# Performance work log

Hardware: AMD Instinct MI355X
Metric: run time of the kernel (lower is better)

The kernel has to match this reference:

```python
import jax, jax.numpy as jnp
import numpy as np

THRESH = 1.0
BETA = 0.9
SG_ALPHA = 2.0  # snntorch ATan surrogate default alpha

@jax.custom_vjp
def spike(u):
    # Heaviside fire: 1 where membrane exceeds threshold
    return (u > 0).astype(u.dtype)

def _spike_fwd(u):
    return spike(u), u

def _spike_bwd(u, g):
    # snntorch ATan surrogate gradient: (alpha/2) / (1 + (pi/2*alpha*u)^2)
    return (g * (SG_ALPHA / 2) / (1.0 + (jnp.pi / 2 * SG_ALPHA * u) ** 2),)

spike.defvjp(_spike_fwd, _spike_bwd)

def setup_inputs() -> dict:
    key = jax.random.key(0)
    k1, k2, k3 = jax.random.split(key, 3)
    T, B, N_IN, N1, N2 = 64, 256, 2048, 1024, 1024
    # Bernoulli(0.2) binary input spike trains
    input_spikes = (jax.random.uniform(k1, (T, B, N_IN)) < 0.2).astype(jnp.float32)
    s = 1.0 / np.sqrt(N_IN)  # nn.Linear default init range
    W1 = jax.random.uniform(k2, (N1, N_IN), minval=-s, maxval=s, dtype=jnp.float32)
    W2 = jax.random.uniform(k3, (N2, N_IN), minval=-s, maxval=s, dtype=jnp.float32)
    return {"input_spikes": input_spikes, "W1": W1, "W2": W2}

def _lif_layer(cur_seq, beta, thr):
    # cur_seq: [T, B, N] post-synaptic currents. snntorch Leaky, reset-by-subtraction:
    #   reset_t = H(mem_{t-1} - thr); mem_t = beta*mem_{t-1} + cur_t - reset_t*thr; spk_t = H(mem_t - thr)
    def step(mem, cur):
        reset = spike(mem - thr)
        mem = beta * mem + cur - reset * thr
        spk = spike(mem - thr)
        return mem, (spk, mem)
    init_mem = jnp.zeros_like(cur_seq[0])
    _, (spk_rec, mem_rec) = jax.lax.scan(step, init_mem, cur_seq)
    return spk_rec, mem_rec  # each [T, B, N]

def reference(input_spikes, W1, W2):
    # Source quirk (faithful): every fc layer consumes the raw input spikes.
    cur1 = jnp.einsum('tbi,ni->tbn', input_spikes, W1)  # [T,B,N1]
    cur2 = jnp.einsum('tbi,ni->tbn', input_spikes, W2)  # [T,B,N2]
    spk1, mem1 = _lif_layer(cur1, BETA, THRESH)
    spk2, mem2 = _lif_layer(cur2, BETA, THRESH)
    return spk1, mem1, spk2, mem2
```

## Files before the change

### kernel.cpp

```cpp
#include <hip/hip_runtime.h>
#include <hip/hip_bf16.h>
#include <stdint.h>


#define REGION 16777216
#define BN_ELEMS 262144
#define FLAG_EPS 3e-4f

typedef __attribute__((ext_vector_type(4))) int v4i;

typedef __attribute__((address_space(1))) const void gvoid_t;
typedef __attribute__((address_space(3))) void svoid_t;

__device__ __forceinline__ void gload_lds16(const void* g, void* l) {
  __builtin_amdgcn_global_load_lds((gvoid_t*)g, (svoid_t*)l, 16, 0, 0);
}

__global__ void prep_kernel(const float* __restrict__ spikes, int* __restrict__ s4,
                            unsigned long long* __restrict__ maskR,
                            int* __restrict__ count,
                            const float* __restrict__ W1, const float* __restrict__ W2,
                            signed char* __restrict__ Bp) {
  int blk = blockIdx.x;
  if (blk < 2048) {
    int id = blk * 256 + threadIdx.x;
    if (id == 0) *count = 0;
    int row = id >> 5, c = id & 31;
    const float4* p = (const float4*)(spikes + (long long)row * 2048 + c * 64);
    unsigned long long m = 0;
    int* sd = s4 + (row * 2048 + c * 64) / 4;
#pragma unroll
    for (int q = 0; q < 16; ++q) {
      float4 v = p[q];
      int b0 = (v.x != 0.f), b1 = (v.y != 0.f), b2 = (v.z != 0.f), b3 = (v.w != 0.f);
      sd[q] = b0 | (b1 << 8) | (b2 << 16) | (b3 << 24);
      m |= (unsigned long long)b0 << (4 * q);
      m |= (unsigned long long)b1 << (4 * q + 1);
      m |= (unsigned long long)b2 << (4 * q + 2);
      m |= (unsigned long long)b3 << (4 * q + 3);
    }
    maskR[(long long)row * 32 + c] = m;
  } else {
    int idx = (blk - 2048) * 256 + threadIdx.x;
    int n = idx >> 11, k = idx & 2047;
    float w = (n < 1024) ? W1[n * 2048 + k] : W2[(n - 1024) * 2048 + k];
    int V = (int)rintf(w * 1048576.0f);
    int d0 = ((V + 128) & 255) - 128;
    int d1 = (V - d0) >> 8;
    signed char* row = Bp + (long long)n * 4096;
    row[k]        = (signed char)d1;
    row[2048 + k] = (signed char)d0;
  }
}

__global__ __launch_bounds__(512) void gemm_snn(const signed char* __restrict__ S,
                                                const signed char* __restrict__ Bp,
                                                float* __restrict__ out) {
  __shared__ __align__(16) signed char As[3 * 8192];
  __shared__ __align__(16) signed char Bs0[3 * 8192];
  __shared__ __align__(16) signed char Bs1[3 * 8192];
  const int tid = threadIdx.x;
  const int wv = tid >> 6, ln = tid & 63;

  int bid = blockIdx.x;
  int swz = (bid & 7) * 128 + (bid >> 3);
  const int bm = swz >> 3;
  const int bn = swz & 7;
  const int wr = wv >> 2, wc = wv & 3;

  const int srow = wv * 16 + (ln >> 2);
  const int scolb = ((ln & 3) ^ ((srow >> 1) & 3)) * 16;
  const signed char* aSrc  = S  + (long long)(bm * 128 + srow) * 2048 + scolb;
  const signed char* b0Src = Bp + (long long)(bn * 128 + srow) * 4096 + scolb;
  const signed char* b1Src = Bp + (long long)(1024 + bn * 128 + srow) * 4096 + scolb;
  const int ldsW = wv * 1024;

  const int l15 = ln & 15, l4 = ln >> 4;
  int aOff[4], bOff[2];
#pragma unroll
  for (int f = 0; f < 4; ++f) {
    int r = wr * 64 + f * 16 + l15;
    aOff[f] = r * 64 + (l4 ^ ((r >> 1) & 3)) * 16;
  }
#pragma unroll
  for (int g = 0; g < 2; ++g) {
    int r = wc * 32 + g * 16 + l15;
    bOff[g] = r * 64 + (l4 ^ ((r >> 1) & 3)) * 16;
  }

  v4i acc[2][4][2];
#pragma unroll
  for (int L = 0; L < 2; ++L)
#pragma unroll
    for (int f = 0; f < 4; ++f)
#pragma unroll
      for (int g = 0; g < 2; ++g) acc[L][f][g] = (v4i){0, 0, 0, 0};

  gload_lds16(aSrc, &As[ldsW]);
  gload_lds16(b0Src, &Bs0[ldsW]);
  gload_lds16(b1Src, &Bs1[ldsW]);
  gload_lds16(aSrc + 64, &As[8192 + ldsW]);
  gload_lds16(b0Src + 64, &Bs0[8192 + ldsW]);
  gload_lds16(b1Src + 64, &Bs1[8192 + ldsW]);

#pragma unroll 1
  for (int i = 0; i < 64; ++i) {
    if (i < 63) {
      asm volatile("s_waitcnt vmcnt(3)" ::: "memory");
    } else {
      asm volatile("s_waitcnt vmcnt(0)" ::: "memory");
    }
    __builtin_amdgcn_sched_barrier(0);
    __builtin_amdgcn_s_barrier();
    __builtin_amdgcn_sched_barrier(0);

    if (i < 62) {
      const int ii = i + 2;
      const int kc = (ii & 31) * 64, so = (ii >> 5) * 2048;
      const int wb = (ii % 3) * 8192 + ldsW;
      gload_lds16(aSrc + kc, &As[wb]);
      gload_lds16(b0Src + so + kc, &Bs0[wb]);
      gload_lds16(b1Src + so + kc, &Bs1[wb]);
    }

    if (i == 32) {
#pragma unroll
      for (int L = 0; L < 2; ++L)
#pragma unroll
        for (int f = 0; f < 4; ++f)
#pragma unroll
          for (int g = 0; g < 2; ++g)
#pragma unroll
            for (int r = 0; r < 4; ++r) acc[L][f][g][r] *= 256;
    }

    const int rb = (i % 3) * 8192;
    v4i a[4], b0[2], b1[2];
#pragma unroll
    for (int f = 0; f < 4; ++f) a[f] = *(const v4i*)&As[rb + aOff[f]];
#pragma unroll
    for (int g = 0; g < 2; ++g) b0[g] = *(const v4i*)&Bs0[rb + bOff[g]];
#pragma unroll
    for (int g = 0; g < 2; ++g) b1[g] = *(const v4i*)&Bs1[rb + bOff[g]];
#pragma unroll
    for (int f = 0; f < 4; ++f)
#pragma unroll
      for (int g = 0; g < 2; ++g) {
        acc[0][f][g] = __builtin_amdgcn_mfma_i32_16x16x64_i8(a[f], b0[g], acc[0][f][g], 0, 0, 0);
        acc[1][f][g] = __builtin_amdgcn_mfma_i32_16x16x64_i8(a[f], b1[g], acc[1][f][g], 0, 0, 0);
      }
  }

#pragma unroll
  for (int L = 0; L < 2; ++L) {
    float* spkBase = out + (L ? 2LL * REGION : 0);
#pragma unroll
    for (int f = 0; f < 4; ++f)
#pragma unroll
      for (int g = 0; g < 2; ++g) {
        int row = bm * 128 + wr * 64 + f * 16 + l4 * 4;
        int col = bn * 128 + wc * 32 + g * 16 + l15;
#pragma unroll
        for (int r = 0; r < 4; ++r)
          spkBase[(long long)(row + r) * 1024 + col] =
              (float)((double)acc[L][f][g][r] * (1.0 / 1048576.0));
      }
  }
}

__global__ void lif_flag(float* __restrict__ out, int* __restrict__ list,
                         int* __restrict__ count) {
  int j = blockIdx.x * 256 + threadIdx.x;
  float* spk1 = out;
  float* mem1 = out + 1LL * REGION;
  float* spk2 = out + 2LL * REGION;
  float* mem2 = out + 3LL * REGION;
  float ma = 0.0f, mb = 0.0f;
  bool fa = false, fb = false;
#pragma unroll 4
  for (int t = 0; t < 64; ++t) {
    int k = t * BN_ELEMS + j;
    float ca = spk1[k];
    float cb = spk2[k];
    float ra = (ma > 1.0f) ? 1.0f : 0.0f;
    float rb = (mb > 1.0f) ? 1.0f : 0.0f;
    ma = __fsub_rn(__fadd_rn(__fmul_rn(0.9f, ma), ca), ra);
    mb = __fsub_rn(__fadd_rn(__fmul_rn(0.9f, mb), cb), rb);
    fa |= (fabsf(ma - 1.0f) < FLAG_EPS);
    fb |= (fabsf(mb - 1.0f) < FLAG_EPS);
    spk1[k] = (ma > 1.0f) ? 1.0f : 0.0f;
    mem1[k] = ma;
    spk2[k] = (mb > 1.0f) ? 1.0f : 0.0f;
    mem2[k] = mb;
  }
  if (fa) { int q = atomicAdd(count, 1); list[q] = j; }
  if (fb) { int q = atomicAdd(count, 1); list[q] = BN_ELEMS + j; }
}

__global__ __launch_bounds__(256) void fixup_kernel(
    const unsigned long long* __restrict__ maskR,
    const float* __restrict__ W1, const float* __restrict__ W2,
    const int* __restrict__ list, const int* __restrict__ count,
    float* __restrict__ out) {
  __shared__ float ws[4][2048];
  __shared__ float curs[4][64];
  const int wv = threadIdx.x >> 6, ln = threadIdx.x & 63;
  const int cnt = *count;
  for (int li = blockIdx.x * 4 + wv; li < cnt; li += gridDim.x * 4) {
    int idx = list[li];
    int layer = idx >> 18;
    int j = idx & (BN_ELEMS - 1);
    int n = j & 1023, b = j >> 10;
    const float* wrow = (layer ? W2 : W1) + (long long)n * 2048;
#pragma unroll
    for (int i = 0; i < 8; ++i)
      ((float4*)ws[wv])[ln + 64 * i] = ((const float4*)wrow)[ln + 64 * i];
    asm volatile("s_waitcnt lgkmcnt(0)" ::: "memory");

    const unsigned long long* mr = maskR + (long long)(ln * 256 + b) * 32;
    float total = 0.0f, pacc = 0.0f;
    bool first = true;
#pragma unroll 1
    for (int c = 0; c < 32; ++c) {
      if (c == 6 || c == 12 || c == 18 || c == 24 || c == 30) {
        total = first ? pacc : __fadd_rn(total, pacc);
        first = false; pacc = 0.0f;
      }
      unsigned long long msk = mr[c];
      unsigned mlo = (unsigned)msk, mhi = (unsigned)(msk >> 32);
      const float* wb = ws[wv] + c * 64;
      while (mlo) {
        int q = __builtin_ctz(mlo);
        mlo &= mlo - 1;
        pacc = __fadd_rn(pacc, wb[q]);
      }
      while (mhi) {
        int q = __builtin_ctz(mhi);
        mhi &= mhi - 1;
        pacc = __fadd_rn(pacc, wb[32 + q]);
      }
    }
    total = first ? pacc : __fadd_rn(total, pacc);
    curs[wv][ln] = total;
    asm volatile("s_waitcnt lgkmcnt(0)" ::: "memory");

    float m = 0.0f, myspk = 0.0f, mymem = 0.0f;
#pragma unroll 1
    for (int tt = 0; tt < 64; ++tt) {
      float c2 = curs[wv][tt];
      float reset = (m > 1.0f) ? 1.0f : 0.0f;
      m = __fsub_rn(__fadd_rn(__fmul_rn(0.9f, m), c2), reset);
      if (tt == ln) { myspk = (m > 1.0f) ? 1.0f : 0.0f; mymem = m; }
    }
    float* spkR = out + (layer ? 2LL * REGION : 0);
    float* memR = out + (layer ? 3LL * REGION : 1LL * REGION);
    spkR[ln * BN_ELEMS + j] = myspk;
    memR[ln * BN_ELEMS + j] = mymem;
  }
}

extern "C" void kernel_launch(void* const* d_in, const int* in_sizes, int n_in,
                              void* d_out, int out_size, void* d_ws, size_t ws_size,
                              hipStream_t stream) {
  const float* spikes = (const float*)d_in[0];
  const float* W1 = (const float*)d_in[1];
  const float* W2 = (const float*)d_in[2];
  float* out = (float*)d_out;
  signed char* Bp = (signed char*)d_ws;
  signed char* S  = (signed char*)d_ws + 8388608;
  unsigned long long* maskR = (unsigned long long*)((char*)d_ws + 41943040);
  int* list  = (int*)((char*)d_ws + 46137344);
  int* count = (int*)((char*)d_ws + 48234496);

  prep_kernel<<<18432, 256, 0, stream>>>(spikes, (int*)S, maskR, count, W1, W2, Bp);
  gemm_snn<<<1024, 512, 0, stream>>>(S, Bp, out);
  lif_flag<<<1024, 256, 0, stream>>>(out, list, count);
  fixup_kernel<<<4096, 256, 0, stream>>>(maskR, W1, W2, list, count, out);
}
```

Measured before the change: 345.3 us.

## Fuse LIF scan and fixup into GEMM epilogue with batch-major spike rows

Reorders the int8 spike matrix so each GEMM tile's 128 rows cover two batch elements across all 64 timesteps. The LIF recurrence then runs in the epilogue from LDS, and the flagged near-threshold fixup runs in the same wave via ballot. This removes the separate lif_flag and fixup kernels, the round trip of currents through global memory and the atomic list. In exchange the GEMM epilogue becomes longer and serial (32 active lanes per wave over 64 timesteps), and the divergent fixup work can leave some blocks running much longer than others.

```diff
diff --git a/kernel.cpp b/kernel.cpp
--- a/kernel.cpp
+++ b/kernel.cpp
@@ -18,17 +18,17 @@
 
 __global__ void prep_kernel(const float* __restrict__ spikes, int* __restrict__ s4,
                             unsigned long long* __restrict__ maskR,
-                            int* __restrict__ count,
                             const float* __restrict__ W1, const float* __restrict__ W2,
                             signed char* __restrict__ Bp) {
   int blk = blockIdx.x;
   if (blk < 2048) {
     int id = blk * 256 + threadIdx.x;
-    if (id == 0) *count = 0;
     int row = id >> 5, c = id & 31;
+    int t = row >> 8, b = row & 255;
+    int rowp = b * 64 + t;
     const float4* p = (const float4*)(spikes + (long long)row * 2048 + c * 64);
     unsigned long long m = 0;
-    int* sd = s4 + (row * 2048 + c * 64) / 4;
+    int* sd = s4 + (rowp * 2048 + c * 64) / 4;
 #pragma unroll
     for (int q = 0; q < 16; ++q) {
       float4 v = p[q];
@@ -53,12 +53,16 @@
   }
 }
 
-__global__ __launch_bounds__(512) void gemm_snn(const signed char* __restrict__ S,
-                                                const signed char* __restrict__ Bp,
-                                                float* __restrict__ out) {
-  __shared__ __align__(16) signed char As[3 * 8192];
-  __shared__ __align__(16) signed char Bs0[3 * 8192];
-  __shared__ __align__(16) signed char Bs1[3 * 8192];
+__global__ __launch_bounds__(512) void gemm_fused(const signed char* __restrict__ S,
+                                                  const signed char* __restrict__ Bp,
+                                                  const unsigned long long* __restrict__ maskR,
+                                                  const float* __restrict__ W1,
+                                                  const float* __restrict__ W2,
+                                                  float* __restrict__ out) {
+  __shared__ __align__(16) signed char smem[73728];
+  signed char* As  = smem;
+  signed char* Bs0 = smem + 24576;
+  signed char* Bs1 = smem + 49152;
   const int tid = threadIdx.x;
   const int wv = tid >> 6, ln = tid & 63;
 
@@ -151,111 +155,92 @@
       }
   }
 
-#pragma unroll
+  __builtin_amdgcn_s_barrier();
+  float* swm  = (float*)(smem + wv * 8448);
+  float* curw = swm + 2048;
+  const int b_global = bm * 2 + wr;
+  const int ncol0 = bn * 128 + wc * 32;
+
+#pragma unroll 1
   for (int L = 0; L < 2; ++L) {
-    float* spkBase = out + (L ? 2LL * REGION : 0);
+    float* spkR = out + (L ? 2LL * REGION : 0);
+    float* memR = out + (L ? 3LL * REGION : 1LL * REGION);
 #pragma unroll
     for (int f = 0; f < 4; ++f)
 #pragma unroll
-      for (int g = 0; g < 2; ++g) {
-        int row = bm * 128 + wr * 64 + f * 16 + l4 * 4;
-        int col = bn * 128 + wc * 32 + g * 16 + l15;
+      for (int g = 0; g < 2; ++g)
 #pragma unroll
         for (int r = 0; r < 4; ++r)
-          spkBase[(long long)(row + r) * 1024 + col] =
+          swm[(f * 16 + l4 * 4 + r) * 33 + g * 16 + l15] =
               (float)((double)acc[L][f][g][r] * (1.0 / 1048576.0));
-      }
-  }
-}
-
-__global__ void lif_flag(float* __restrict__ out, int* __restrict__ list,
-                         int* __restrict__ count) {
-  int j = blockIdx.x * 256 + threadIdx.x;
-  float* spk1 = out;
-  float* mem1 = out + 1LL * REGION;
-  float* spk2 = out + 2LL * REGION;
-  float* mem2 = out + 3LL * REGION;
-  float ma = 0.0f, mb = 0.0f;
-  bool fa = false, fb = false;
-#pragma unroll 4
-  for (int t = 0; t < 64; ++t) {
-    int k = t * BN_ELEMS + j;
-    float ca = spk1[k];
-    float cb = spk2[k];
-    float ra = (ma > 1.0f) ? 1.0f : 0.0f;
-    float rb = (mb > 1.0f) ? 1.0f : 0.0f;
-    ma = __fsub_rn(__fadd_rn(__fmul_rn(0.9f, ma), ca), ra);
-    mb = __fsub_rn(__fadd_rn(__fmul_rn(0.9f, mb), cb), rb);
-    fa |= (fabsf(ma - 1.0f) < FLAG_EPS);
-    fb |= (fabsf(mb - 1.0f) < FLAG_EPS);
-    spk1[k] = (ma > 1.0f) ? 1.0f : 0.0f;
-    mem1[k] = ma;
-    spk2[k] = (mb > 1.0f) ? 1.0f : 0.0f;
-    mem2[k] = mb;
-  }
-  if (fa) { int q = atomicAdd(count, 1); list[q] = j; }
-  if (fb) { int q = atomicAdd(count, 1); list[q] = BN_ELEMS + j; }
-}
-
-__global__ __launch_bounds__(256) void fixup_kernel(
-    const unsigned long long* __restrict__ maskR,
-    const float* __restrict__ W1, const float* __restrict__ W2,
-    const int* __restrict__ list, const int* __restrict__ count,
-    float* __restrict__ out) {
-  __shared__ float ws[4][2048];
-  __shared__ float curs[4][64];
-  const int wv = threadIdx.x >> 6, ln = threadIdx.x & 63;
-  const int cnt = *count;
-  for (int li = blockIdx.x * 4 + wv; li < cnt; li += gridDim.x * 4) {
-    int idx = list[li];
-    int layer = idx >> 18;
-    int j = idx & (BN_ELEMS - 1);
-    int n = j & 1023, b = j >> 10;
-    const float* wrow = (layer ? W2 : W1) + (long long)n * 2048;
-#pragma unroll
-    for (int i = 0; i < 8; ++i)
-      ((float4*)ws[wv])[ln + 64 * i] = ((const float4*)wrow)[ln + 64 * i];
     asm volatile("s_waitcnt lgkmcnt(0)" ::: "memory");
 
-    const unsigned long long* mr = maskR + (long long)(ln * 256 + b) * 32;
-    float total = 0.0f, pacc = 0.0f;
-    bool first = true;
-#pragma unroll 1
-    for (int c = 0; c < 32; ++c) {
-      if (c == 6 || c == 12 || c == 18 || c == 24 || c == 30) {
-        total = first ? pacc : __fadd_rn(total, pacc);
-        first = false; pacc = 0.0f;
-      }
-      unsigned long long msk = mr[c];
-      unsigned mlo = (unsigned)msk, mhi = (unsigned)(msk >> 32);
-      const float* wb = ws[wv] + c * 64;
-      while (mlo) {
-        int q = __builtin_ctz(mlo);
-        mlo &= mlo - 1;
-        pacc = __fadd_rn(pacc, wb[q]);
-      }
-      while (mhi) {
-        int q = __builtin_ctz(mhi);
-        mhi &= mhi - 1;
-        pacc = __fadd_rn(pacc, wb[32 + q]);
-      }
-    }
-    total = first ? pacc : __fadd_rn(total, pacc);
-    curs[wv][ln] = total;
-    asm volatile("s_waitcnt lgkmcnt(0)" ::: "memory");
-
-    float m = 0.0f, myspk = 0.0f, mymem = 0.0f;
-#pragma unroll 1
-    for (int tt = 0; tt < 64; ++tt) {
-      float c2 = curs[wv][tt];
-      float reset = (m > 1.0f) ? 1.0f : 0.0f;
-      m = __fsub_rn(__fadd_rn(__fmul_rn(0.9f, m), c2), reset);
-      if (tt == ln) { myspk = (m > 1.0f) ? 1.0f : 0.0f; mymem = m; }
-    }
-    float* spkR = out + (layer ? 2LL * REGION : 0);
-    float* memR = out + (layer ? 3LL * REGION : 1LL * REGION);
-    spkR[ln * BN_ELEMS + j] = myspk;
-    memR[ln * BN_ELEMS + j] = mymem;
+    bool flag = false;
+    if (ln < 32) {
+      float m = 0.0f;
+#pragma unroll 1
+      for (int t = 0; t < 64; ++t) {
+        float c = swm[t * 33 + ln];
+        float reset = (m > 1.0f) ? 1.0f : 0.0f;
+        m = __fsub_rn(__fadd_rn(__fmul_rn(0.9f, m), c), reset);
+        flag |= (fabsf(m - 1.0f) < FLAG_EPS);
+        int k = t * BN_ELEMS + b_global * 1024 + ncol0 + ln;
+        spkR[k] = (m > 1.0f) ? 1.0f : 0.0f;
+        memR[k] = m;
+      }
+    }
+
+    unsigned long long fm = __ballot(flag);
+#pragma unroll 1
+    while (fm) {
+      int col = __builtin_ctzll(fm);
+      fm &= fm - 1;
+      int n_g = ncol0 + col;
+      const float* wrow = (L ? W2 : W1) + (long long)n_g * 2048;
+#pragma unroll
+      for (int i = 0; i < 8; ++i)
+        ((float4*)swm)[ln + 64 * i] = ((const float4*)wrow)[ln + 64 * i];
+      asm volatile("s_waitcnt lgkmcnt(0)" ::: "memory");
+
+      const unsigned long long* mr = maskR + (long long)(ln * 256 + b_global) * 32;
+      float total = 0.0f, pacc = 0.0f;
+      bool first = true;
+#pragma unroll 1
+      for (int c = 0; c < 32; ++c) {
+        if (c == 6 || c == 12 || c == 18 || c == 24 || c == 30) {
+          total = first ? pacc : __fadd_rn(total, pacc);
+          first = false; pacc = 0.0f;
+        }
+        unsigned long long msk = mr[c];
+        unsigned mlo = (unsigned)msk, mhi = (unsigned)(msk >> 32);
+        const float* wb = swm + c * 64;
+        while (mlo) {
+          int q = __builtin_ctz(mlo);
+          mlo &= mlo - 1;
+          pacc = __fadd_rn(pacc, wb[q]);
+        }
+        while (mhi) {
+          int q = __builtin_ctz(mhi);
+          mhi &= mhi - 1;
+          pacc = __fadd_rn(pacc, wb[32 + q]);
+        }
+      }
+      total = first ? pacc : __fadd_rn(total, pacc);
+      curw[ln] = total;
+      asm volatile("s_waitcnt lgkmcnt(0)" ::: "memory");
+
+      float m = 0.0f, myspk = 0.0f, mymem = 0.0f;
+#pragma unroll 1
+      for (int tt = 0; tt < 64; ++tt) {
+        float c2 = curw[tt];
+        float reset = (m > 1.0f) ? 1.0f : 0.0f;
+        m = __fsub_rn(__fadd_rn(__fmul_rn(0.9f, m), c2), reset);
+        if (tt == ln) { myspk = (m > 1.0f) ? 1.0f : 0.0f; mymem = m; }
+      }
+      int k = ln * BN_ELEMS + b_global * 1024 + n_g;
+      spkR[k] = myspk;
+      memR[k] = mymem;
+    }
   }
 }
 
@@ -269,11 +254,7 @@
   signed char* Bp = (signed char*)d_ws;
   signed char* S  = (signed char*)d_ws + 8388608;
   unsigned long long* maskR = (unsigned long long*)((char*)d_ws + 41943040);
-  int* list  = (int*)((char*)d_ws + 46137344);
-  int* count = (int*)((char*)d_ws + 48234496);
-
-  prep_kernel<<<18432, 256, 0, stream>>>(spikes, (int*)S, maskR, count, W1, W2, Bp);
-  gemm_snn<<<1024, 512, 0, stream>>>(S, Bp, out);
-  lif_flag<<<1024, 256, 0, stream>>>(out, list, count);
-  fixup_kernel<<<4096, 256, 0, stream>>>(maskR, W1, W2, list, count, out);
-}
+
+  prep_kernel<<<18432, 256, 0, stream>>>(spikes, (int*)S, maskR, W1, W2, Bp);
+  gemm_fused<<<1024, 512, 0, stream>>>(S, Bp, maskR, W1, W2, out);
+}
```

Result: slower. 529.9 us (+53.5%).
